# Optimization experiments

Hardware: AMD Instinct MI355X
Metric: run time of the kernel (lower is better)

## Reference

```python
import jax, jax.numpy as jnp
import numpy as np

B, LQ, LK, H = 4, 512, 512, 128


def _orthogonal(key, n, dtype=jnp.float32):
    a = jax.random.normal(key, (n, n), dtype=dtype)
    q, r = jnp.linalg.qr(a)
    return q * jnp.sign(jnp.diag(r))[None, :]


def setup_inputs() -> dict:
    key = jax.random.key(0)
    kq, kk, ku, kt, kb, kw, kwb = jax.random.split(key, 7)
    queries = jax.random.normal(kq, (B, LQ, H), dtype=jnp.float32)
    keys = jax.random.normal(kk, (B, LK, H), dtype=jnp.float32)
    U = _orthogonal(ku, H)
    T = _orthogonal(kt, H)
    b = jax.random.uniform(kb, (H,), minval=-0.1, maxval=0.1, dtype=jnp.float32)
    # nn.Linear(H, 1): weight (1, H), bias (1,); kaiming-uniform-ish init bound
    bound = 1.0 / np.sqrt(H)
    w = jax.random.uniform(kw, (H,), minval=-bound, maxval=bound, dtype=jnp.float32)
    w_bias = jax.random.uniform(kwb, (), minval=-bound, maxval=bound, dtype=jnp.float32)
    return {"queries": queries, "keys": keys, "U": U, "T": T, "b": b, "w": w, "w_bias": w_bias}


def reference(queries, keys, U, T, b, w, w_bias):
    # qU: (B, Lq, H), kT: (B, Lk, H)
    qU = jnp.einsum('bqh,hd->bqd', queries, U)
    kT = jnp.einsum('bkh,hd->bkd', keys, T)
    # broadcast sum -> (B, Lk, Lq, H), tanh, reduce with Linear(H,1)
    s = qU[:, None, :, :] + kT[:, :, None, :] + b
    scores = jnp.einsum('bkqh,h->bkq', jnp.tanh(s), w) + w_bias
    return scores.transpose(0, 2, 1)  # (B, Lq, Lk)
```

## Files before the change

### kernel.cpp

```cpp
#include <hip/hip_runtime.h>

#define B_   4
#define LQ_  512
#define LK_  512
#define H_   128

#define RPB  4
#define QPT  4
#define KTH  256


__global__ __launch_bounds__(128) void proj_kernel(
    const float* __restrict__ queries, const float* __restrict__ keys,
    const float* __restrict__ U, const float* __restrict__ T,
    const float* __restrict__ bvec, const float* __restrict__ w,
    const float* __restrict__ wb,
    float* __restrict__ Eq, float* __restrict__ Ek, float* __restrict__ base)
{
    const int side = blockIdx.y;
    const float* __restrict__ X = side ? keys : queries;
    const float* __restrict__ M = side ? T : U;
    float* __restrict__ Y       = side ? Ek : Eq;

    const int t  = threadIdx.x;
    const int r0 = blockIdx.x * RPB;

    if (side == 1 && blockIdx.x == 0 && t == 0) {
        float s = wb[0];
        for (int h = 0; h < H_; ++h) s += w[h];
        base[0] = s;
    }

    float acc[RPB];
#pragma unroll
    for (int i = 0; i < RPB; ++i) acc[i] = 0.f;

#pragma unroll 8
    for (int d = 0; d < H_; ++d) {
        float m = M[d * H_ + t];
#pragma unroll
        for (int i = 0; i < RPB; ++i)
            acc[i] = fmaf(X[(size_t)(r0 + i) * H_ + d], m, acc[i]);
    }

    const float C = 2.8853900817779268f;
    const float bb = side ? bvec[t] : 0.f;
#pragma unroll
    for (int i = 0; i < RPB; ++i)
        Y[(size_t)(r0 + i) * H_ + t] =
            __builtin_amdgcn_exp2f(C * (acc[i] + bb));
}

__global__ __launch_bounds__(KTH) void score_kernel(
    const float* __restrict__ Eq, const float* __restrict__ Ek,
    const float* __restrict__ w, const float* __restrict__ base_p,
    float* __restrict__ out)
{
    const int b  = blockIdx.z;
    const int q0 = blockIdx.y * QPT;
    const int k  = blockIdx.x * KTH + threadIdx.x;

    const float* __restrict__ eqr = Eq + ((size_t)b * LQ_ + q0) * H_;
    const float* __restrict__ ekr = Ek + ((size_t)b * LK_ + k) * H_;

    float acc[QPT];
#pragma unroll
    for (int i = 0; i < QPT; ++i) acc[i] = 0.f;

#pragma unroll 4
    for (int c = 0; c < H_; c += 4) {
        float4 ek4 = *(const float4*)(ekr + c);
        float w0 = w[c], w1 = w[c + 1], w2 = w[c + 2], w3 = w[c + 3];
#pragma unroll
        for (int q = 0; q < QPT; ++q) {
            const float* eq = eqr + q * H_ + c;
            float x0 = fmaf(eq[0], ek4.x, 1.f);
            float x1 = fmaf(eq[1], ek4.y, 1.f);
            float x2 = fmaf(eq[2], ek4.z, 1.f);
            float x3 = fmaf(eq[3], ek4.w, 1.f);
            float d01 = x0 * x1;
            float d23 = x2 * x3;
            float n01 = fmaf(w1, x0, w0 * x1);
            float n23 = fmaf(w3, x2, w2 * x3);
            float num = fmaf(n23, d01, n01 * d23);
            float den = d01 * d23;
            acc[q] = fmaf(num, __builtin_amdgcn_rcpf(den), acc[q]);
        }
    }

    const float base = base_p[0];
#pragma unroll
    for (int q = 0; q < QPT; ++q)
        out[((size_t)b * LQ_ + q0 + q) * LK_ + k] = fmaf(-2.f, acc[q], base);
}

extern "C" void kernel_launch(void* const* d_in, const int* in_sizes, int n_in,
                              void* d_out, int out_size, void* d_ws, size_t ws_size,
                              hipStream_t stream)
{
    const float* queries = (const float*)d_in[0];
    const float* keys    = (const float*)d_in[1];
    const float* U       = (const float*)d_in[2];
    const float* T       = (const float*)d_in[3];
    const float* bvec    = (const float*)d_in[4];
    const float* w       = (const float*)d_in[5];
    const float* wb      = (const float*)d_in[6];
    float* out = (float*)d_out;

    float* Eq   = (float*)d_ws;
    float* Ek   = Eq + (size_t)B_ * LQ_ * H_;
    float* base = Ek + (size_t)B_ * LK_ * H_;

    proj_kernel<<<dim3((B_ * LQ_) / RPB, 2), 128, 0, stream>>>(
        queries, keys, U, T, bvec, w, wb, Eq, Ek, base);

    score_kernel<<<dim3(LK_ / KTH, LQ_ / QPT, B_), KTH, 0, stream>>>(
        Eq, Ek, w, base, out);
}
```

Before: 92.77 us.

## Store key projections in interleaved transposed layout and double queries per thread

The key projection is now written as [b][h/4][k][4], so adjacent threads in the score kernel read consecutive float4s and the loads coalesce instead of striding by 512 bytes per thread. The score kernel also processes 8 queries per thread instead of 4, which halves the grid's y-dimension and reuses each loaded key vector across more queries. The inner unroll drops from 4 to 2 to limit register pressure. The projection kernel's key-side stores become scattered in exchange.

```diff
diff --git a/kernel.cpp b/kernel.cpp
--- a/kernel.cpp
+++ b/kernel.cpp
@@ -6,7 +6,7 @@
 #define H_   128
 
 #define RPB  4
-#define QPT  4
+#define QPT  8
 #define KTH  256
 
 
@@ -15,12 +15,11 @@
     const float* __restrict__ U, const float* __restrict__ T,
     const float* __restrict__ bvec, const float* __restrict__ w,
     const float* __restrict__ wb,
-    float* __restrict__ Eq, float* __restrict__ Ek, float* __restrict__ base)
+    float* __restrict__ Eq, float* __restrict__ EkT, float* __restrict__ base)
 {
     const int side = blockIdx.y;
     const float* __restrict__ X = side ? keys : queries;
     const float* __restrict__ M = side ? T : U;
-    float* __restrict__ Y       = side ? Ek : Eq;
 
     const int t  = threadIdx.x;
     const int r0 = blockIdx.x * RPB;
@@ -44,15 +43,26 @@
     }
 
     const float C = 2.8853900817779268f;
-    const float bb = side ? bvec[t] : 0.f;
+    if (side) {
+        const int b     = r0 / LK_;
+        const int kbase = r0 % LK_;
+        const float bb  = bvec[t];
+        float* __restrict__ y = EkT + (size_t)b * H_ * LK_
+                              + (size_t)(t >> 2) * (LK_ * 4) + (t & 3);
 #pragma unroll
-    for (int i = 0; i < RPB; ++i)
-        Y[(size_t)(r0 + i) * H_ + t] =
-            __builtin_amdgcn_exp2f(C * (acc[i] + bb));
+        for (int i = 0; i < RPB; ++i)
+            y[(size_t)(kbase + i) * 4] =
+                __builtin_amdgcn_exp2f(C * (acc[i] + bb));
+    } else {
+#pragma unroll
+        for (int i = 0; i < RPB; ++i)
+            Eq[(size_t)(r0 + i) * H_ + t] =
+                __builtin_amdgcn_exp2f(C * acc[i]);
+    }
 }
 
 __global__ __launch_bounds__(KTH) void score_kernel(
-    const float* __restrict__ Eq, const float* __restrict__ Ek,
+    const float* __restrict__ Eq, const float* __restrict__ EkT,
     const float* __restrict__ w, const float* __restrict__ base_p,
     float* __restrict__ out)
 {
@@ -61,15 +71,15 @@
     const int k  = blockIdx.x * KTH + threadIdx.x;
 
     const float* __restrict__ eqr = Eq + ((size_t)b * LQ_ + q0) * H_;
-    const float* __restrict__ ekr = Ek + ((size_t)b * LK_ + k) * H_;
+    const float* __restrict__ ekT = EkT + (size_t)b * H_ * LK_ + (size_t)k * 4;
 
     float acc[QPT];
 #pragma unroll
     for (int i = 0; i < QPT; ++i) acc[i] = 0.f;
 
-#pragma unroll 4
+#pragma unroll 2
     for (int c = 0; c < H_; c += 4) {
-        float4 ek4 = *(const float4*)(ekr + c);
+        float4 ek4 = *(const float4*)(ekT + (size_t)(c >> 2) * (LK_ * 4));
         float w0 = w[c], w1 = w[c + 1], w2 = w[c + 2], w3 = w[c + 3];
 #pragma unroll
         for (int q = 0; q < QPT; ++q) {
@@ -108,12 +118,12 @@
     float* out = (float*)d_out;
 
     float* Eq   = (float*)d_ws;
-    float* Ek   = Eq + (size_t)B_ * LQ_ * H_;
-    float* base = Ek + (size_t)B_ * LK_ * H_;
+    float* EkT  = Eq + (size_t)B_ * LQ_ * H_;
+    float* base = EkT + (size_t)B_ * LK_ * H_;
 
     proj_kernel<<<dim3((B_ * LQ_) / RPB, 2), 128, 0, stream>>>(
-        queries, keys, U, T, bvec, w, wb, Eq, Ek, base);
+        queries, keys, U, T, bvec, w, wb, Eq, EkT, base);
 
     score_kernel<<<dim3(LK_ / KTH, LQ_ / QPT, B_), KTH, 0, stream>>>(
-        Eq, Ek, w, base, out);
+        Eq, EkT, w, base, out);
 }
```

Result: no change. 91.32 us (-1.6%).
